# Optimization experiments

Hardware: AMD Instinct MI355X
Metric: run time of the kernel (lower is better)

The kernel has to match this reference:

```python
import jax, jax.numpy as jnp
import numpy as np

D_MODEL = 1024
NUM_HEADS = 16
MAX_LEN = 2048
D_HEAD = D_MODEL // NUM_HEADS
BATCH = 2
SEQ = 2048


def setup_inputs() -> dict:
    key = jax.random.key(0)
    ks = jax.random.split(key, 8)
    s = 1.0 / np.sqrt(D_MODEL)
    return {
        "x": jax.random.normal(ks[0], (BATCH, SEQ, D_MODEL), dtype=jnp.float32),
        "Wq": jax.random.uniform(ks[1], (D_MODEL, D_MODEL), jnp.float32, -s, s),
        "bq": jax.random.uniform(ks[2], (D_MODEL,), jnp.float32, -s, s),
        "Wk": jax.random.uniform(ks[3], (D_MODEL, D_MODEL), jnp.float32, -s, s),
        "bk": jax.random.uniform(ks[4], (D_MODEL,), jnp.float32, -s, s),
        "Wv": jax.random.uniform(ks[5], (D_MODEL, D_MODEL), jnp.float32, -s, s),
        "bv": jax.random.uniform(ks[6], (D_MODEL,), jnp.float32, -s, s),
        "Er": jax.random.normal(ks[7], (MAX_LEN, D_HEAD), dtype=jnp.float32),
    }


def _skew(QEr):
    # QEr: [B, H, S, S]  (music-transformer skew trick)
    B, H, S, _ = QEr.shape
    padded = jnp.pad(QEr, ((0, 0), (0, 0), (0, 0), (1, 0)))  # [B,H,S,S+1]
    reshaped = padded.reshape(B, H, S + 1, S)
    return reshaped[:, :, 1:, :]  # [B,H,S,S]


def reference(x, Wq, bq, Wk, bk, Wv, bv, Er):
    B, S, D = x.shape
    H, Dh = NUM_HEADS, D_HEAD
    # projections (torch Linear: x @ W.T + b)
    q = (jnp.einsum('bsd,ed->bse', x, Wq) + bq).reshape(B, S, H, Dh).transpose(0, 2, 1, 3)
    k = (jnp.einsum('bsd,ed->bse', x, Wk) + bk).reshape(B, S, H, Dh).transpose(0, 2, 1, 3)
    v = (jnp.einsum('bsd,ed->bse', x, Wv) + bv).reshape(B, S, H, Dh).transpose(0, 2, 1, 3)
    # relative position scores
    Er_slice = Er[MAX_LEN - S:, :]                    # [S, Dh]
    QEr = jnp.einsum('bhsd,td->bhst', q, Er_slice)    # [B,H,S,S]
    Srel = _skew(QEr)
    QKt = jnp.einsum('bhsd,bhtd->bhst', q, k)
    attn = (QKt + Srel) / jnp.sqrt(jnp.asarray(Dh, x.dtype))
    causal = jnp.tril(jnp.ones((S, S), dtype=bool))
    attn = jnp.where(causal[None, None], attn, -jnp.inf)
    attn = jax.nn.softmax(attn, axis=-1)
    out = jnp.einsum('bhst,bhtd->bhsd', attn, v)      # [B,H,S,Dh]
    out = out.transpose(0, 2, 1, 3).reshape(B, S, D)
    return out  # dropout is identity in eval mode
```

## Files before the change

### kernel.cpp

```cpp
#include <hip/hip_runtime.h>
#include <hip/hip_bf16.h>

constexpr int B  = 2;
constexpr int S  = 2048;
constexpr int D  = 1024;
constexpr int H  = 16;

typedef unsigned short u16t;
typedef unsigned long long u64;
typedef __attribute__((ext_vector_type(8))) short short8;
typedef __attribute__((ext_vector_type(4))) float float4v;

__device__ __forceinline__ float b2f(unsigned int u) {
    union { unsigned int i; float f; } c; c.i = u << 16; return c.f;
}
__device__ __forceinline__ u16t f2b(float f) {
    __hip_bfloat16 h = __float2bfloat16(f);
    union { __hip_bfloat16 h; u16t u; } c; c.h = h; return c.u;
}
__device__ __forceinline__ unsigned int pkbf(float a, float b) {
    return (unsigned int)f2b(a) | ((unsigned int)f2b(b) << 16);
}
__device__ __forceinline__ u64 pack4(float4 v) {
    return (u64)f2b(v.x) | ((u64)f2b(v.y) << 16) | ((u64)f2b(v.z) << 32) | ((u64)f2b(v.w) << 48);
}

typedef __attribute__((address_space(1))) const unsigned int* as1_u32p;
typedef __attribute__((address_space(3))) unsigned int* as3_u32p;
__device__ __forceinline__ void gll16(const void* g, void* l) {
    __builtin_amdgcn_global_load_lds((as1_u32p)g, (as3_u32p)l, 16, 0, 0);
}

constexpr size_t XB_OFF = 0;
constexpr size_t WQ_OFF = 4194304;
constexpr size_t WK_OFF = 5242880;
constexpr size_t WV_OFF = 6291456;
constexpr size_t ER_OFF = 7340032;
constexpr size_t QW_OFF = 7471104;
constexpr size_t KW_OFF = 11665408;
constexpr size_t VT_OFF = 15859712;

__global__ __launch_bounds__(256) void prep_bf16(
    const float* __restrict__ x,  const float* __restrict__ Wq,
    const float* __restrict__ Wk, const float* __restrict__ Wv,
    const float* __restrict__ Er, u64* __restrict__ dst)
{
    size_t i4 = (size_t)blockIdx.x * 256 + threadIdx.x;
    const float* src; size_t off;
    if      (i4 < 1048576) { src = x;  off = i4; }
    else if (i4 < 1310720) { src = Wq; off = i4 - 1048576; }
    else if (i4 < 1572864) { src = Wk; off = i4 - 1310720; }
    else if (i4 < 1835008) { src = Wv; off = i4 - 1572864; }
    else                   { src = Er; off = i4 - 1835008; }
    float4 v = ((const float4*)src)[off];
    __builtin_nontemporal_store(pack4(v), &dst[i4]);
}

__global__ __launch_bounds__(256, 3) void qkv_mfma(
    const u16t* __restrict__ xb,
    const u16t* __restrict__ wqb, const u16t* __restrict__ wkb, const u16t* __restrict__ wvb,
    const float* __restrict__ bq, const float* __restrict__ bk, const float* __restrict__ bv,
    u16t* __restrict__ qo, u16t* __restrict__ ko, u16t* __restrict__ vT)
{
    const int z = blockIdx.z;
    const u16t*  W    = (z == 0) ? wqb : (z == 1) ? wkb : wvb;
    const float* bias = (z == 0) ? bq  : (z == 1) ? bk  : bv;

    __shared__ __align__(16) u16t SMEM[2 * 128 * 64];
    char* XsB = (char*)SMEM;
    char* WsB = XsB + 16384;

    const int tid = threadIdx.x;
    const int w = tid >> 6, lane = tid & 63;
    const int quad = lane >> 4, l16 = lane & 15;
    const int m0 = blockIdx.x * 128, n0 = blockIdx.y * 128;
    const int mi = (w >> 1) * 64, ni = (w & 1) * 64;

    const int srow = lane >> 3;
    const int d8s  = (lane & 7) ^ (srow & 7);
    const int xk   = l16 & 7;

    float4v acc[4][4];
    #pragma unroll
    for (int mt = 0; mt < 4; ++mt)
        #pragma unroll
        for (int nt = 0; nt < 4; ++nt) acc[mt][nt] = (float4v){0.f, 0.f, 0.f, 0.f};

    for (int k0 = 0; k0 < D; k0 += 64) {
        #pragma unroll
        for (int it = 0; it < 4; ++it) {
            int ci  = w * 4 + it;
            int row = ci * 8 + srow;
            gll16(&xb[(size_t)(m0 + row) * D + k0 + d8s * 8], XsB + ci * 1024);
            gll16(&W [(size_t)(n0 + row) * D + k0 + d8s * 8], WsB + ci * 1024);
        }
        __syncthreads();

        short8 af[4][2], bf[4][2];
        #pragma unroll
        for (int mt = 0; mt < 4; ++mt) {
            int r = mi + mt * 16 + l16;
            af[mt][0] = *(const short8*)(XsB + r * 128 + ((quad       ^ xk) << 4));
            af[mt][1] = *(const short8*)(XsB + r * 128 + (((quad + 4) ^ xk) << 4));
        }
        #pragma unroll
        for (int nt = 0; nt < 4; ++nt) {
            int r = ni + nt * 16 + l16;
            bf[nt][0] = *(const short8*)(WsB + r * 128 + ((quad       ^ xk) << 4));
            bf[nt][1] = *(const short8*)(WsB + r * 128 + (((quad + 4) ^ xk) << 4));
        }
        #pragma unroll
        for (int mt = 0; mt < 4; ++mt)
            #pragma unroll
            for (int nt = 0; nt < 4; ++nt) {
                acc[mt][nt] = __builtin_amdgcn_mfma_f32_16x16x32_bf16(af[mt][0], bf[nt][0], acc[mt][nt], 0, 0, 0);
                acc[mt][nt] = __builtin_amdgcn_mfma_f32_16x16x32_bf16(af[mt][1], bf[nt][1], acc[mt][nt], 0, 0, 0);
            }
        __syncthreads();
    }

    float bias_v[4];
    #pragma unroll
    for (int nt = 0; nt < 4; ++nt) bias_v[nt] = bias[n0 + ni + nt * 16 + l16];
    #pragma unroll
    for (int mt = 0; mt < 4; ++mt)
        #pragma unroll
        for (int nt = 0; nt < 4; ++nt)
            #pragma unroll
            for (int rg = 0; rg < 4; ++rg) acc[mt][nt][rg] += bias_v[nt];

    const int hB = n0 >> 6;
    const int b_ = m0 >> 11;
    const int sB = m0 & (S - 1);
    char* EP = (char*)SMEM;

    if (z < 2) {
        u16t* outp = (z == 0) ? qo : ko;
        #pragma unroll 1
        for (int hp = 0; hp < 2; ++hp) {
            __syncthreads();
            if ((w & 1) == hp) {
                #pragma unroll
                for (int mt = 0; mt < 4; ++mt)
                    #pragma unroll
                    for (int nt = 0; nt < 4; ++nt) {
                        int col = nt * 16 + l16;
                        #pragma unroll
                        for (int rg = 0; rg < 4; ++rg) {
                            int row = mi + mt * 16 + quad * 4 + rg;
                            *(u16t*)(EP + row * 144 + col * 2) = f2b(acc[mt][nt][rg]);
                        }
                    }
            }
            __syncthreads();
            #pragma unroll
            for (int it = 0; it < 4; ++it) {
                int idx = tid + it * 256;
                int row = idx >> 3, c8 = idx & 7;
                short8 vv = *(const short8*)(EP + row * 144 + c8 * 16);
                __builtin_nontemporal_store(vv,
                    (short8*)&outp[((size_t)(b_ * H + hB + hp) * S + sB + row) * 64 + c8 * 8]);
            }
        }
    } else {
        #pragma unroll 1
        for (int hp = 0; hp < 2; ++hp) {
            __syncthreads();
            if ((w & 1) == hp) {
                #pragma unroll
                for (int mt = 0; mt < 4; ++mt)
                    #pragma unroll
                    for (int nt = 0; nt < 4; ++nt) {
                        int rowD = nt * 16 + l16;
                        #pragma unroll
                        for (int rg = 0; rg < 4; ++rg) {
                            int colS = mi + mt * 16 + quad * 4 + rg;
                            *(u16t*)(EP + rowD * 272 + colS * 2) = f2b(acc[mt][nt][rg]);
                        }
                    }
            }
            __syncthreads();
            #pragma unroll
            for (int it = 0; it < 4; ++it) {
                int idx = tid + it * 256;
                int rowD = idx >> 4, c16 = idx & 15;
                short8 vv = *(const short8*)(EP + rowD * 272 + c16 * 16);
                __builtin_nontemporal_store(vv,
                    (short8*)&vT[((size_t)(b_ * H + hB + hp) * 64 + rowD) * S + sB + c16 * 8]);
            }
        }
    }
}

__global__ __launch_bounds__(256, 4) void attn_mfma(
    const u16t* __restrict__ q, const u16t* __restrict__ k,
    const u16t* __restrict__ vT, const u16t* __restrict__ er,
    float* __restrict__ out)
{
    __shared__ __align__(16) u16t KsS[2][64 * 64];
    __shared__ __align__(16) u16t VsS[2][64 * 64];
    __shared__ __align__(16) u16t PsS[64 * 64];
    char* KsB = (char*)KsS;
    char* VsB = (char*)VsS;
    char* PsB = (char*)PsS;
    float* lrows = (float*)PsS;

    const int tid = threadIdx.x;
    const int w = tid >> 6, lane = tid & 63;
    const int quad = lane >> 4, l16 = lane & 15;

    const int r_  = blockIdx.x;
    const int g   = blockIdx.y;
    const int bh  = r_ & 31;
    const int slot = r_ >> 5;
    const int ix  = (g == 0) ? (31 - slot)
                  : (g == 1) ? (16 + slot)
                  : (g == 2) ? (15 - slot)
                  :            slot;
    const int hh = bh & (H - 1), bb = bh >> 4;

    const u16t* qb = q  + (size_t)bh * S * 64;
    const u16t* kb = k  + (size_t)bh * S * 64;
    const u16t* vb = vT + (size_t)bh * 64 * S;

    const int xk = (l16 & 7);
    const float SC = 0.18033688f;
    const float M2 = 17.3125f;

    const int srow = lane >> 3;
    const int d8s  = (lane & 7) ^ (srow & 7);

    const int s0 = ix * 64;

    const size_t qoff = (size_t)(s0 + w * 16 + l16) * 64;
    const short8 Qa0 = *(const short8*)&qb[qoff + quad * 8];
    const short8 Qa1 = *(const short8*)&qb[qoff + 32 + quad * 8];

    float4v accO[4], L[5];
    #pragma unroll
    for (int t = 0; t < 4; ++t) accO[t] = (float4v){0.f, 0.f, 0.f, 0.f};
    float lsum[4] = {0.f, 0.f, 0.f, 0.f};

    #pragma unroll
    for (int it = 0; it < 2; ++it) {
        int ci = w * 2 + it;
        int prow = ci * 8 + srow;
        gll16(&kb[(size_t)prow * 64 + d8s * 8], KsB + ci * 1024);
        gll16(&vb[(size_t)prow * S + d8s * 8], VsB + ci * 1024);
    }
    __syncthreads();

    for (int jt = 0; jt <= ix; ++jt) {
        const int t0 = jt * 64;
        const int jbase = S - 64 - s0 + t0;
        const bool diag = (jt == ix);
        const int bsel = (jt & 1) * 8192;

        short8 ef0[4], ef1[4], e00, e01;
        #pragma unroll
        for (int c = 1; c <= 4; ++c) {
            int grow = jbase + (3 - w + c) * 16 + l16;
            if (grow > S - 1) grow = S - 1;
            const u16t* ep = &er[(size_t)grow * 64 + quad * 8];
            ef0[c - 1] = *(const short8*)ep;
            ef1[c - 1] = *(const short8*)(ep + 32);
        }
        if (jt == 0) {
            int grow = jbase + (3 - w) * 16 + l16;
            if (grow > S - 1) grow = S - 1;
            const u16t* ep = &er[(size_t)grow * 64 + quad * 8];
            e00 = *(const short8*)ep;
            e01 = *(const short8*)(ep + 32);
        }

        if (jt < ix) {
            int nb = ((jt + 1) & 1) * 8192;
            #pragma unroll
            for (int it = 0; it < 2; ++it) {
                int ci = w * 2 + it;
                int prow = ci * 8 + srow;
                gll16(&kb[(size_t)(t0 + 64 + prow) * 64 + d8s * 8], KsB + nb + ci * 1024);
                gll16(&vb[(size_t)prow * S + t0 + 64 + d8s * 8], VsB + nb + ci * 1024);
            }
        }

        float4v S1[4];
        #pragma unroll
        for (int nt = 0; nt < 4; ++nt) {
            int row = nt * 16 + l16;
            short8 b0 = *(const short8*)(KsB + bsel + row * 128 + ((quad ^ xk) << 4));
            short8 b1 = *(const short8*)(KsB + bsel + row * 128 + (((quad + 4) ^ xk) << 4));
            float4v a = (float4v){0.f, 0.f, 0.f, 0.f};
            a = __builtin_amdgcn_mfma_f32_16x16x32_bf16(Qa0, b0, a, 0, 0, 0);
            a = __builtin_amdgcn_mfma_f32_16x16x32_bf16(Qa1, b1, a, 0, 0, 0);
            S1[nt] = a;
        }

        if (jt == 0) {
            float4v e = (float4v){0.f, 0.f, 0.f, 0.f};
            e = __builtin_amdgcn_mfma_f32_16x16x32_bf16(Qa0, e00, e, 0, 0, 0);
            e = __builtin_amdgcn_mfma_f32_16x16x32_bf16(Qa1, e01, e, 0, 0, 0);
            L[0] = e;
        } else {
            L[0] = L[4];
        }
        #pragma unroll
        for (int c = 1; c <= 4; ++c) {
            float4v e = (float4v){0.f, 0.f, 0.f, 0.f};
            e = __builtin_amdgcn_mfma_f32_16x16x32_bf16(Qa0, ef0[c - 1], e, 0, 0, 0);
            e = __builtin_amdgcn_mfma_f32_16x16x32_bf16(Qa1, ef1[c - 1], e, 0, 0, 0);
            L[c] = e;
        }

#define SM_BODY(DIAGC)                                                        \
        _Pragma("unroll")                                                     \
        for (int rg = 0; rg < 4; ++rg) {                                      \
            const int usel = quad * 4 + rg;                                   \
            const int thr = 15 - usel;                                        \
            const int sidx = ((lane & 48) | ((l16 + thr) & 15)) * 4;          \
            const bool give_lo = (l16 >= thr);                                \
            unsigned int p01 = give_lo ? pkbf(L[0][rg], L[1][rg]) : pkbf(L[1][rg], L[2][rg]); \
            unsigned int p23 = give_lo ? pkbf(L[2][rg], L[3][rg]) : pkbf(L[3][rg], L[4][rg]); \
            unsigned int q01 = (unsigned int)__builtin_amdgcn_ds_bpermute(sidx, (int)p01); \
            unsigned int q23 = (unsigned int)__builtin_amdgcn_ds_bpermute(sidx, (int)p23); \
            float qe[4] = { b2f(q01 & 0xffffu), b2f(q01 >> 16),               \
                            b2f(q23 & 0xffffu), b2f(q23 >> 16) };             \
            const int i_ = w * 16 + usel;                                     \
            const int ikey = i_ & 7;                                          \
            float psum = 0.f;                                                 \
            _Pragma("unroll")                                                 \
            for (int nt = 0; nt < 4; ++nt) {                                  \
                float s2 = fmaf(S1[nt][rg] + qe[nt], SC, -M2);                \
                float p = exp2f(s2);                                          \
                if (DIAGC) p = (nt * 16 + l16 > i_) ? 0.f : p;                \
                psum += p;                                                    \
                int j_ = nt * 16 + l16;                                       \
                *(u16t*)(PsB + i_ * 128 + (((j_ >> 3) ^ ikey) << 4) + (j_ & 7) * 2) = f2b(p); \
            }                                                                 \
            lsum[rg] += psum;                                                 \
        }
        if (diag) { SM_BODY(true) } else { SM_BODY(false) }
#undef SM_BODY

        {
            int ar = w * 16 + l16;
            short8 pa0 = *(const short8*)(PsB + ar * 128 + ((quad ^ (ar & 7)) << 4));
            short8 pa1 = *(const short8*)(PsB + ar * 128 + (((quad + 4) ^ (ar & 7)) << 4));
            #pragma unroll
            for (int td = 0; td < 4; ++td) {
                int row = td * 16 + l16;
                short8 a0 = *(const short8*)(VsB + bsel + row * 128 + ((quad ^ xk) << 4));
                short8 a1 = *(const short8*)(VsB + bsel + row * 128 + (((quad + 4) ^ xk) << 4));
                accO[td] = __builtin_amdgcn_mfma_f32_16x16x32_bf16(a0, pa0, accO[td], 0, 0, 0);
                accO[td] = __builtin_amdgcn_mfma_f32_16x16x32_bf16(a1, pa1, accO[td], 0, 0, 0);
            }
        }
        __syncthreads();
    }

    #pragma unroll
    for (int rg = 0; rg < 4; ++rg) {
        float s = lsum[rg];
        s += __shfl_xor(s, 1);
        s += __shfl_xor(s, 2);
        s += __shfl_xor(s, 4);
        s += __shfl_xor(s, 8);
        if (l16 == 0) lrows[w * 16 + quad * 4 + rg] = s;
    }
    float inv = 1.f / lrows[w * 16 + l16];

    float* ob = out + (size_t)bb * S * D + (size_t)hh * 64
                + (size_t)(s0 + w * 16 + l16) * D;
    #pragma unroll
    for (int td = 0; td < 4; ++td) {
        float4 o;
        o.x = accO[td][0] * inv;
        o.y = accO[td][1] * inv;
        o.z = accO[td][2] * inv;
        o.w = accO[td][3] * inv;
        *(float4*)&ob[td * 16 + quad * 4] = o;
    }
}

extern "C" void kernel_launch(void* const* d_in, const int* in_sizes, int n_in,
                              void* d_out, int out_size, void* d_ws, size_t ws_size,
                              hipStream_t stream) {
    const float* x  = (const float*)d_in[0];
    const float* Wq = (const float*)d_in[1];
    const float* bq = (const float*)d_in[2];
    const float* Wk = (const float*)d_in[3];
    const float* bk = (const float*)d_in[4];
    const float* Wv = (const float*)d_in[5];
    const float* bv = (const float*)d_in[6];
    const float* Er = (const float*)d_in[7];
    float* out = (float*)d_out;

    u16t* ws16 = (u16t*)d_ws;
    u16t* xb  = ws16 + XB_OFF;
    u16t* wqb = ws16 + WQ_OFF;
    u16t* wkb = ws16 + WK_OFF;
    u16t* wvb = ws16 + WV_OFF;
    u16t* erb = ws16 + ER_OFF;
    u16t* qw  = ws16 + QW_OFF;
    u16t* kw  = ws16 + KW_OFF;
    u16t* vTw = ws16 + VT_OFF;

    prep_bf16<<<dim3(7296), dim3(256), 0, stream>>>(x, Wq, Wk, Wv, Er, (u64*)d_ws);

    qkv_mfma<<<dim3(32, 8, 3), dim3(256), 0, stream>>>(
        xb, wqb, wkb, wvb, bq, bk, bv, qw, kw, vTw);

    attn_mfma<<<dim3(256, 4), dim3(256), 0, stream>>>(qw, kw, vTw, erb, out);
}
```

Measured before the change: 237.6 us.

## Remap block IDs for XCD locality, drop nontemporal stores, add MFMA priority

Both GEMM and attention grids become 1D, and the block index is remapped so consecutive logical tiles (same weight or same batch-head) land on the same XCD. The aim is to improve L2 reuse across MI355X's chiplets. Nontemporal stores of intermediate bf16 buffers are replaced with normal stores so consumer kernels can hit in cache. s_setprio is raised around the MFMA sections of the attention loop to favour matrix issue over softmax waves.

```diff
diff --git a/kernel.cpp b/kernel.cpp
--- a/kernel.cpp
+++ b/kernel.cpp
@@ -53,7 +53,7 @@
     else if (i4 < 1835008) { src = Wv; off = i4 - 1572864; }
     else                   { src = Er; off = i4 - 1835008; }
     float4 v = ((const float4*)src)[off];
-    __builtin_nontemporal_store(pack4(v), &dst[i4]);
+    dst[i4] = pack4(v);
 }
 
 __global__ __launch_bounds__(256, 3) void qkv_mfma(
@@ -62,7 +62,12 @@
     const float* __restrict__ bq, const float* __restrict__ bk, const float* __restrict__ bv,
     u16t* __restrict__ qo, u16t* __restrict__ ko, u16t* __restrict__ vT)
 {
-    const int z = blockIdx.z;
+    const int hwid = blockIdx.x;
+    const int L    = (hwid & 7) * 96 + (hwid >> 3);
+    const int mblk = L & 31;
+    const int nblk = (L >> 5) & 7;
+    const int z    = L >> 8;
+
     const u16t*  W    = (z == 0) ? wqb : (z == 1) ? wkb : wvb;
     const float* bias = (z == 0) ? bq  : (z == 1) ? bk  : bv;
 
@@ -73,7 +78,7 @@
     const int tid = threadIdx.x;
     const int w = tid >> 6, lane = tid & 63;
     const int quad = lane >> 4, l16 = lane & 15;
-    const int m0 = blockIdx.x * 128, n0 = blockIdx.y * 128;
+    const int m0 = mblk * 128, n0 = nblk * 128;
     const int mi = (w >> 1) * 64, ni = (w & 1) * 64;
 
     const int srow = lane >> 3;
@@ -158,8 +163,7 @@
                 int idx = tid + it * 256;
                 int row = idx >> 3, c8 = idx & 7;
                 short8 vv = *(const short8*)(EP + row * 144 + c8 * 16);
-                __builtin_nontemporal_store(vv,
-                    (short8*)&outp[((size_t)(b_ * H + hB + hp) * S + sB + row) * 64 + c8 * 8]);
+                *(short8*)&outp[((size_t)(b_ * H + hB + hp) * S + sB + row) * 64 + c8 * 8] = vv;
             }
         }
     } else {
@@ -185,8 +189,7 @@
                 int idx = tid + it * 256;
                 int rowD = idx >> 4, c16 = idx & 15;
                 short8 vv = *(const short8*)(EP + rowD * 272 + c16 * 16);
-                __builtin_nontemporal_store(vv,
-                    (short8*)&vT[((size_t)(b_ * H + hB + hp) * 64 + rowD) * S + sB + c16 * 8]);
+                *(short8*)&vT[((size_t)(b_ * H + hB + hp) * 64 + rowD) * S + sB + c16 * 8] = vv;
             }
         }
     }
@@ -209,10 +212,12 @@
     const int w = tid >> 6, lane = tid & 63;
     const int quad = lane >> 4, l16 = lane & 15;
 
-    const int r_  = blockIdx.x;
-    const int g   = blockIdx.y;
-    const int bh  = r_ & 31;
-    const int slot = r_ >> 5;
+    const int hwid = blockIdx.x;
+    const int L_   = (hwid & 7) * 128 + (hwid >> 3);
+    const int bh   = L_ >> 5;
+    const int rest = L_ & 31;
+    const int g    = rest >> 3;
+    const int slot = rest & 7;
     const int ix  = (g == 0) ? (31 - slot)
                   : (g == 1) ? (16 + slot)
                   : (g == 2) ? (15 - slot)
@@ -284,6 +289,7 @@
             }
         }
 
+        __builtin_amdgcn_s_setprio(1);
         float4v S1[4];
         #pragma unroll
         for (int nt = 0; nt < 4; ++nt) {
@@ -311,6 +317,7 @@
             e = __builtin_amdgcn_mfma_f32_16x16x32_bf16(Qa1, ef1[c - 1], e, 0, 0, 0);
             L[c] = e;
         }
+        __builtin_amdgcn_s_setprio(0);
 
 #define SM_BODY(DIAGC)                                                        \
         _Pragma("unroll")                                                     \
@@ -343,6 +350,7 @@
 #undef SM_BODY
 
         {
+            __builtin_amdgcn_s_setprio(1);
             int ar = w * 16 + l16;
             short8 pa0 = *(const short8*)(PsB + ar * 128 + ((quad ^ (ar & 7)) << 4));
             short8 pa1 = *(const short8*)(PsB + ar * 128 + (((quad + 4) ^ (ar & 7)) << 4));
@@ -354,6 +362,7 @@
                 accO[td] = __builtin_amdgcn_mfma_f32_16x16x32_bf16(a0, pa0, accO[td], 0, 0, 0);
                 accO[td] = __builtin_amdgcn_mfma_f32_16x16x32_bf16(a1, pa1, accO[td], 0, 0, 0);
             }
+            __builtin_amdgcn_s_setprio(0);
         }
         __syncthreads();
     }
@@ -407,8 +416,8 @@
 
     prep_bf16<<<dim3(7296), dim3(256), 0, stream>>>(x, Wq, Wk, Wv, Er, (u64*)d_ws);
 
-    qkv_mfma<<<dim3(32, 8, 3), dim3(256), 0, stream>>>(
+    qkv_mfma<<<dim3(768), dim3(256), 0, stream>>>(
         xb, wqb, wkb, wvb, bq, bk, bv, qw, kw, vTw);
 
-    attn_mfma<<<dim3(256, 4), dim3(256), 0, stream>>>(qw, kw, vTw, erb, out);
-}
+    attn_mfma<<<dim3(1024), dim3(256), 0, stream>>>(qw, kw, vTw, erb, out);
+}
```

After: 298.3 us. 1.26x slower.
